# Optimization experiments

Measured on AMD Instinct MI355X. Metric: run time of the kernel, lower is better.

## Reference

```python
import jax, jax.numpy as jnp
import numpy as np

B, S, D, H, DK, FF = 2, 2048, 1024, 16, 64, 4096
EPS = 1e-6


def _layernorm(x, g, b):
    m = jnp.mean(x, axis=-1, keepdims=True)
    v = jnp.mean((x - m) ** 2, axis=-1, keepdims=True)
    return (x - m) * jax.lax.rsqrt(v + EPS) * g + b


def setup_inputs() -> dict:
    key = jax.random.key(0)
    ks = jax.random.split(key, 20)
    sc = 0.02
    rn = lambda k, sh: (jax.random.normal(k, sh, jnp.float32) * sc)
    return {
        "inputs": jax.random.normal(ks[0], (B, S, D), jnp.float32),
        "wq": rn(ks[1], (D, H * DK)), "bq": jnp.zeros((H * DK,), jnp.float32),
        "wk": rn(ks[2], (D, H * DK)), "bk": jnp.zeros((H * DK,), jnp.float32),
        "wv": rn(ks[3], (D, H * DK)), "bv": jnp.zeros((H * DK,), jnp.float32),
        "wo": rn(ks[4], (H * DK, D)), "bo": jnp.zeros((D,), jnp.float32),
        "ln1_g": jnp.ones((D,), jnp.float32), "ln1_b": jnp.zeros((D,), jnp.float32),
        "wi0": rn(ks[5], (D, FF)), "bi0": jnp.zeros((FF,), jnp.float32),
        "wi1": rn(ks[6], (D, FF)), "bi1": jnp.zeros((FF,), jnp.float32),
        "wff": rn(ks[7], (FF, D)), "bff": jnp.zeros((D,), jnp.float32),
        "ln2_g": jnp.ones((D,), jnp.float32), "ln2_b": jnp.zeros((D,), jnp.float32),
    }


def reference(inputs, wq, bq, wk, bk, wv, bv, wo, bo, ln1_g, ln1_b,
              wi0, bi0, wi1, bi1, wff, bff, ln2_g, ln2_b):
    # --- pre-norm MHA block ---
    h = _layernorm(inputs, ln1_g, ln1_b)
    q = (h @ wq + bq).reshape(B, S, H, DK)
    k = (h @ wk + bk).reshape(B, S, H, DK)
    v = (h @ wv + bv).reshape(B, S, H, DK)
    scores = jnp.einsum('bqhd,bkhd->bhqk', q, k) / jnp.sqrt(jnp.float32(DK))
    attn = jax.nn.softmax(scores, axis=-1)                 # [B,H,S,S]
    ctx = jnp.einsum('bhqk,bkhd->bqhd', attn, v).reshape(B, S, H * DK)
    h1 = inputs + (ctx @ wo + bo)
    # --- pre-norm GeGLU FFN block ---
    h2 = _layernorm(h1, ln2_g, ln2_b)
    hg = jax.nn.gelu(h2 @ wi0 + bi0, approximate=False)
    hl = h2 @ wi1 + bi1
    out = h1 + ((hg * hl) @ wff + bff)
    return out, attn
```

## Files before the change

### kernel.cpp

```cpp
#include <hip/hip_runtime.h>
#include <hip/hip_bf16.h>
#include <cstdint>

#define DEV __device__ __forceinline__

typedef __bf16 bf16_t;
typedef __bf16 bf16x8 __attribute__((ext_vector_type(8)));
typedef __bf16 bf16x4 __attribute__((ext_vector_type(4)));
typedef float  f32x4  __attribute__((ext_vector_type(4)));

constexpr int Bb = 2, Ss = 2048, Dd = 1024, Hh = 16, DKk = 64, FFf = 4096;
constexpr int TOK = Bb * Ss;
constexpr float LN_EPS = 1e-6f;

DEV void g2l16(const void* g, void* l) {
    __builtin_amdgcn_global_load_lds(
        (const __attribute__((address_space(1))) unsigned int*)g,
        (__attribute__((address_space(3))) unsigned int*)l, 16, 0, 0);
}

#define WAITCNT(N) asm volatile("s_waitcnt vmcnt(" #N ")" ::: "memory")
#define SCHEDB() __builtin_amdgcn_sched_barrier(0)

__global__ __launch_bounds__(256)
void transpose_all(const float* __restrict__ wq, const float* __restrict__ wk,
                   const float* __restrict__ wv, const float* __restrict__ wo,
                   const float* __restrict__ wi0, const float* __restrict__ wi1,
                   const float* __restrict__ wff,
                   bf16_t* wqT, bf16_t* wkT, bf16_t* wvT, bf16_t* woT,
                   bf16_t* wi0T, bf16_t* wi1T, bf16_t* wffT) {
    __shared__ float t[32][33];
    const int id = blockIdx.x;
    const float* src; bf16_t* dst; int K, N, tt;
    if (id < 4096) {
        const int w = id >> 10; tt = id & 1023; K = 1024; N = 1024;
        src = w == 0 ? wq : w == 1 ? wk : w == 2 ? wv : wo;
        dst = w == 0 ? wqT : w == 1 ? wkT : w == 2 ? wvT : woT;
    } else if (id < 12288) {
        const int w = (id - 4096) >> 12; tt = (id - 4096) & 4095; K = 1024; N = 4096;
        src = w ? wi1 : wi0; dst = w ? wi1T : wi0T;
    } else {
        tt = id - 12288; K = 4096; N = 1024;
        src = wff; dst = wffT;
    }
    const int ntn = N >> 5;
    const int n0 = (tt % ntn) * 32, k0 = (tt / ntn) * 32;
    const int tx = threadIdx.x & 31, ty = threadIdx.x >> 5;
#pragma unroll
    for (int i = 0; i < 4; ++i)
        t[ty + 8 * i][tx] = src[(size_t)(k0 + ty + 8 * i) * N + n0 + tx];
    __syncthreads();
#pragma unroll
    for (int i = 0; i < 4; ++i)
        dst[(size_t)(n0 + ty + 8 * i) * K + k0 + tx] = (bf16_t)t[tx][ty + 8 * i];
}

__global__ __launch_bounds__(256)
void concat3(const float* __restrict__ a, const float* __restrict__ b,
             const float* __restrict__ c, float* __restrict__ o) {
    const int i = blockIdx.x * 256 + threadIdx.x;
    o[i] = a[i]; o[1024 + i] = b[i]; o[2048 + i] = c[i];
}

__global__ __launch_bounds__(256)
void ln_fwd(const float* __restrict__ x, const float* __restrict__ g,
            const float* __restrict__ b, bf16_t* __restrict__ out) {
    __shared__ float red[8];
    const int row = blockIdx.x, tid = threadIdx.x;
    const float4 v = ((const float4*)(x + (size_t)row * Dd))[tid];
    float s  = v.x + v.y + v.z + v.w;
    float sq = v.x * v.x + v.y * v.y + v.z * v.z + v.w * v.w;
#pragma unroll
    for (int o = 32; o; o >>= 1) { s += __shfl_xor(s, o); sq += __shfl_xor(sq, o); }
    if ((tid & 63) == 0) { red[tid >> 6] = s; red[4 + (tid >> 6)] = sq; }
    __syncthreads();
    s  = red[0] + red[1] + red[2] + red[3];
    sq = red[4] + red[5] + red[6] + red[7];
    const float mean = s * (1.f / Dd);
    const float var  = sq * (1.f / Dd) - mean * mean;
    const float rs   = rsqrtf(var + LN_EPS);
    const float4 gv = ((const float4*)g)[tid];
    const float4 bv = ((const float4*)b)[tid];
    bf16x4 o4;
    o4[0] = (bf16_t)((v.x - mean) * rs * gv.x + bv.x);
    o4[1] = (bf16_t)((v.y - mean) * rs * gv.y + bv.y);
    o4[2] = (bf16_t)((v.z - mean) * rs * gv.z + bv.z);
    o4[3] = (bf16_t)((v.w - mean) * rs * gv.w + bv.w);
    ((bf16x4*)(out + (size_t)row * Dd))[tid] = o4;
}

template <int EPI>
DEV void gemm_epi(float val, int gr, int gc, int N,
                  void* outp, void* out2, void* out3, const float* resid) {
    if constexpr (EPI == 0) {
        ((bf16_t*)outp)[(size_t)gr * N + gc] = (bf16_t)val;
    } else if constexpr (EPI == 1) {
        const size_t idx = (size_t)gr * N + gc;
        ((float*)outp)[idx] = val + resid[idx];
    } else {
        const int sel = gc >> 10, col = gc & 1023;
        if (sel == 0) {
            ((bf16_t*)outp)[(size_t)gr * 1024 + col] = (bf16_t)val;
        } else if (sel == 1) {
            ((bf16_t*)out2)[(size_t)gr * 1024 + col] = (bf16_t)val;
        } else {
            const int bb = gr >> 11, sS = gr & 2047;
            ((bf16_t*)out3)[((size_t)bb << 21) + ((size_t)col << 11) + sS] = (bf16_t)val;
        }
    }
}

template <int BM, int BN, int EPI>
__global__ __launch_bounds__(256)
void gemm_t(const bf16_t* __restrict__ A, const bf16_t* __restrict__ Bt,
            const float* __restrict__ bias, const float* __restrict__ resid,
            void* __restrict__ outp, void* __restrict__ out2,
            void* __restrict__ out3, int M, int N, int K) {
    constexpr int WM = BM / 2, WN = BN / 2;
    constexpr int MI = WM / 16, NI = WN / 16;
    constexpr int CA = BM / 32, CB = BN / 32;
    __shared__ bf16_t As[BM * 64];
    __shared__ bf16_t Bs[BN * 64];
    const int tid = threadIdx.x;
    const int lane = tid & 63;
    const int wave = tid >> 6;
    const int wr = wave >> 1, wc = wave & 1;
    const int m0 = blockIdx.y * BM, n0 = blockIdx.x * BN;
    const int lr = lane & 15, lg = lane >> 4;

    const f32x4 z0 = {0.f, 0.f, 0.f, 0.f};
    f32x4 acc[MI][NI];
#pragma unroll
    for (int i = 0; i < MI; ++i)
#pragma unroll
        for (int j = 0; j < NI; ++j) acc[i][j] = z0;

    for (int k0 = 0; k0 < K; k0 += 64) {
#pragma unroll
        for (int c = 0; c < CA; ++c) {
            const int lin = c * 256 + tid;
            const int row = lin >> 3, col = (lin & 7) * 8;
            g2l16(A + (size_t)(m0 + row) * K + k0 + col, (char*)As + lin * 16);
        }
#pragma unroll
        for (int c = 0; c < CB; ++c) {
            const int lin = c * 256 + tid;
            const int row = lin >> 3, col = (lin & 7) * 8;
            g2l16(Bt + (size_t)(n0 + row) * K + k0 + col, (char*)Bs + lin * 16);
        }
        __syncthreads();

        bf16x8 af[2][MI], bw[2][NI];
#pragma unroll
        for (int kk = 0; kk < 2; ++kk)
#pragma unroll
            for (int mi = 0; mi < MI; ++mi)
                af[kk][mi] = *(const bf16x8*)(As + (wr * WM + mi * 16 + lr) * 64 +
                                              kk * 32 + lg * 8);
#pragma unroll
        for (int kk = 0; kk < 2; ++kk)
#pragma unroll
            for (int ni = 0; ni < NI; ++ni)
                bw[kk][ni] = *(const bf16x8*)(Bs + (wc * WN + ni * 16 + lr) * 64 +
                                              kk * 32 + lg * 8);
#pragma unroll
        for (int mi = 0; mi < MI; ++mi)
#pragma unroll
            for (int ni = 0; ni < NI; ++ni) {
                acc[mi][ni] = __builtin_amdgcn_mfma_f32_16x16x32_bf16(
                    af[0][mi], bw[0][ni], acc[mi][ni], 0, 0, 0);
                acc[mi][ni] = __builtin_amdgcn_mfma_f32_16x16x32_bf16(
                    af[1][mi], bw[1][ni], acc[mi][ni], 0, 0, 0);
            }
        __syncthreads();
    }

#pragma unroll
    for (int mi = 0; mi < MI; ++mi)
#pragma unroll
        for (int ni = 0; ni < NI; ++ni) {
            const int gc = n0 + wc * WN + ni * 16 + lr;
            const int gr0 = m0 + wr * WM + mi * 16 + lg * 4;
            const float bvl = bias[gc];
#pragma unroll
            for (int r = 0; r < 4; ++r)
                gemm_epi<EPI>(acc[mi][ni][r] + bvl, gr0 + r, gc, N, outp, out2, out3, resid);
        }
}

__global__ __launch_bounds__(256)
void gemm_geglu(const bf16_t* __restrict__ A, const bf16_t* __restrict__ Bg,
                const bf16_t* __restrict__ Bl, const float* __restrict__ bi0,
                const float* __restrict__ bi1, bf16_t* __restrict__ gout) {
    __shared__ bf16_t As[128 * 64];
    __shared__ bf16_t Bgs[64 * 64];
    __shared__ bf16_t Bls[64 * 64];
    const int tid = threadIdx.x;
    const int lane = tid & 63;
    const int wave = tid >> 6;
    const int wr = wave >> 1, wc = wave & 1;
    const int m0 = blockIdx.y * 128, n0 = blockIdx.x * 64;
    const int lr = lane & 15, lg = lane >> 4;

    const f32x4 z0 = {0.f, 0.f, 0.f, 0.f};
    f32x4 ag[4][2], al[4][2];
#pragma unroll
    for (int i = 0; i < 4; ++i)
#pragma unroll
        for (int j = 0; j < 2; ++j) { ag[i][j] = z0; al[i][j] = z0; }

    for (int k0 = 0; k0 < 1024; k0 += 64) {
#pragma unroll
        for (int c = 0; c < 4; ++c) {
            const int lin = c * 256 + tid;
            const int row = lin >> 3, col = (lin & 7) * 8;
            g2l16(A + (size_t)(m0 + row) * 1024 + k0 + col, (char*)As + lin * 16);
        }
#pragma unroll
        for (int c = 0; c < 2; ++c) {
            const int lin = c * 256 + tid;
            const int row = lin >> 3, col = (lin & 7) * 8;
            g2l16(Bg + (size_t)(n0 + row) * 1024 + k0 + col, (char*)Bgs + lin * 16);
        }
#pragma unroll
        for (int c = 0; c < 2; ++c) {
            const int lin = c * 256 + tid;
            const int row = lin >> 3, col = (lin & 7) * 8;
            g2l16(Bl + (size_t)(n0 + row) * 1024 + k0 + col, (char*)Bls + lin * 16);
        }
        __syncthreads();

        bf16x8 af[2][4], bg[2][2], bl[2][2];
#pragma unroll
        for (int kk = 0; kk < 2; ++kk) {
#pragma unroll
            for (int mi = 0; mi < 4; ++mi)
                af[kk][mi] = *(const bf16x8*)(As + (wr * 64 + mi * 16 + lr) * 64 +
                                              kk * 32 + lg * 8);
#pragma unroll
            for (int ni = 0; ni < 2; ++ni) {
                bg[kk][ni] = *(const bf16x8*)(Bgs + (wc * 32 + ni * 16 + lr) * 64 +
                                              kk * 32 + lg * 8);
                bl[kk][ni] = *(const bf16x8*)(Bls + (wc * 32 + ni * 16 + lr) * 64 +
                                              kk * 32 + lg * 8);
            }
        }
#pragma unroll
        for (int mi = 0; mi < 4; ++mi)
#pragma unroll
            for (int ni = 0; ni < 2; ++ni) {
#pragma unroll
                for (int kk = 0; kk < 2; ++kk) {
                    ag[mi][ni] = __builtin_amdgcn_mfma_f32_16x16x32_bf16(
                        af[kk][mi], bg[kk][ni], ag[mi][ni], 0, 0, 0);
                    al[mi][ni] = __builtin_amdgcn_mfma_f32_16x16x32_bf16(
                        af[kk][mi], bl[kk][ni], al[mi][ni], 0, 0, 0);
                }
            }
        __syncthreads();
    }

#pragma unroll
    for (int mi = 0; mi < 4; ++mi)
#pragma unroll
        for (int ni = 0; ni < 2; ++ni) {
            const int gc = n0 + wc * 32 + ni * 16 + lr;
            const int gr0 = m0 + wr * 64 + mi * 16 + lg * 4;
            const float b0 = bi0[gc], b1 = bi1[gc];
#pragma unroll
            for (int r = 0; r < 4; ++r) {
                const float x = ag[mi][ni][r] + b0;
                const float y = al[mi][ni][r] + b1;
                const float ge = 0.5f * x * (1.f + erff(x * 0.70710678118654752f));
                gout[(size_t)(gr0 + r) * 4096 + gc] = (bf16_t)(ge * y);
            }
        }
}

__global__ __launch_bounds__(256)
void attn_fused(const bf16_t* __restrict__ q, const bf16_t* __restrict__ k,
                const bf16_t* __restrict__ vT, float* __restrict__ attn,
                bf16_t* __restrict__ ctx) {
    __shared__ bf16_t Ks[3][64 * 64];
    __shared__ bf16_t Vs[3][64 * 64];
    const int tid = threadIdx.x, lane = tid & 63, wave = tid >> 6;
    const int lr = lane & 15, lg = lane >> 4;
    int blk = blockIdx.x;
    blk = (blk & 7) * 128 + (blk >> 3);
    const int qc = blk & 31, bh = blk >> 5;
    const int b = bh >> 4, h = bh & 15;
    const int q0 = qc * 64 + wave * 16;
    const size_t base = (size_t)b * (Ss * 1024) + h * 64;
    constexpr float SCL = 0.125f * 1.4426950408889634f;
    const f32x4 z0 = {0.f, 0.f, 0.f, 0.f};

    const int st_r8 = lane >> 3;
    const int st_c0 = (lane & 7) ^ (st_r8 & 3);

    const bf16x8 aq0 = *(const bf16x8*)(q + base + (size_t)(q0 + lr) * 1024 + lg * 8);
    const bf16x8 aq1 = *(const bf16x8*)(q + base + (size_t)(q0 + lr) * 1024 + 32 + lg * 8);
    const bf16_t* kb = k + base;
    const bf16_t* vb_base = vT + ((size_t)bh * 64) * Ss;

#define STAGE_K(kt_, buf_)                                                        \
    {                                                                             \
        _Pragma("unroll")                                                         \
        for (int i = 0; i < 2; ++i)                                               \
            g2l16(kb + (size_t)((kt_) * 64 + wave * 16 + i * 8 + st_r8) * 1024 +  \
                      (st_c0 ^ (i * 4)) * 8,                                      \
                  &Ks[buf_][wave * 1024 + i * 512]);                              \
    }
#define STAGE_V(kt_, buf_)                                                        \
    {                                                                             \
        _Pragma("unroll")                                                         \
        for (int i = 0; i < 2; ++i)                                               \
            g2l16(vb_base + (size_t)(wave * 16 + i * 8 + st_r8) * Ss +            \
                      (kt_) * 64 + (st_c0 ^ (i * 4)) * 8,                         \
                  &Vs[buf_][wave * 1024 + i * 512]);                              \
    }

    f32x4 ea = z0, eb = z0;
    STAGE_K(0, 0);
    STAGE_K(1, 1);
    for (int kt = 0; kt < 32; ++kt) {
        const int buf = kt % 3;
        if (kt == 31) { WAITCNT(0); } else { WAITCNT(2); }
        SCHEDB();
        __builtin_amdgcn_s_barrier();
        SCHEDB();
        f32x4 sa[4];
        __builtin_amdgcn_s_setprio(1);
#pragma unroll
        for (int ct = 0; ct < 4; ++ct) {
            const int ar = ct * 16 + lr;
            const int hz = (ar & 3) | (((ar >> 3) & 1) << 2);
            bf16x8 k0 = *(const bf16x8*)&Ks[buf][ar * 64 + (lg ^ hz) * 8];
            bf16x8 k1 = *(const bf16x8*)&Ks[buf][ar * 64 + (((4 + lg) ^ hz)) * 8];
            sa[ct] = __builtin_amdgcn_mfma_f32_16x16x32_bf16(k0, aq0, z0, 0, 0, 0);
            sa[ct] = __builtin_amdgcn_mfma_f32_16x16x32_bf16(k1, aq1, sa[ct], 0, 0, 0);
        }
        __builtin_amdgcn_s_setprio(0);
#pragma unroll
        for (int r = 0; r < 4; ++r) {
            ea[r] += exp2f(sa[0][r] * SCL) + exp2f(sa[1][r] * SCL);
            eb[r] += exp2f(sa[2][r] * SCL) + exp2f(sa[3][r] * SCL);
        }
        if (kt + 2 < 32) STAGE_K(kt + 2, (kt + 2) % 3);
    }
    float e = ((ea[0] + ea[1]) + (ea[2] + ea[3])) + ((eb[0] + eb[1]) + (eb[2] + eb[3]));
    e += __shfl_xor(e, 16);
    e += __shfl_xor(e, 32);
    const float invl = 1.f / e;

    f32x4 cacc[4];
#pragma unroll
    for (int nd = 0; nd < 4; ++nd) cacc[nd] = z0;

    float* attn_base = attn + ((size_t)bh * Ss + q0 + lr) * Ss;

    __builtin_amdgcn_s_barrier();
    SCHEDB();

    STAGE_K(0, 0); STAGE_V(0, 0);
    STAGE_K(1, 1); STAGE_V(1, 1);
    for (int kt = 0; kt < 32; ++kt) {
        const int buf = kt % 3;
        if (kt == 0 || kt == 31) { WAITCNT(4); } else { WAITCNT(8); }
        SCHEDB();
        __builtin_amdgcn_s_barrier();
        SCHEDB();
#pragma unroll
        for (int kp = 0; kp < 2; ++kp) {
            bf16x8 pa;
            __builtin_amdgcn_s_setprio(1);
#pragma unroll
            for (int ch = 0; ch < 2; ++ch) {
                const int pr = kp * 32 + (lr >> 2) * 8 + ch * 4 + (lr & 3);
                const int hz = (pr & 3) | (((pr >> 3) & 1) << 2);
                bf16x8 k0 = *(const bf16x8*)&Ks[buf][pr * 64 + (lg ^ hz) * 8];
                bf16x8 k1 = *(const bf16x8*)&Ks[buf][pr * 64 + (((4 + lg) ^ hz)) * 8];
                f32x4 sb = __builtin_amdgcn_mfma_f32_16x16x32_bf16(k0, aq0, z0, 0, 0, 0);
                sb = __builtin_amdgcn_mfma_f32_16x16x32_bf16(k1, aq1, sb, 0, 0, 0);
                float4 p;
                p.x = exp2f(sb[0] * SCL) * invl;
                p.y = exp2f(sb[1] * SCL) * invl;
                p.z = exp2f(sb[2] * SCL) * invl;
                p.w = exp2f(sb[3] * SCL) * invl;
                *(float4*)(attn_base + kt * 64 + kp * 32 + lg * 8 + ch * 4) = p;
                pa[ch * 4 + 0] = (bf16_t)p.x;
                pa[ch * 4 + 1] = (bf16_t)p.y;
                pa[ch * 4 + 2] = (bf16_t)p.z;
                pa[ch * 4 + 3] = (bf16_t)p.w;
            }
#pragma unroll
            for (int nd = 0; nd < 4; ++nd) {
                const int vr = nd * 16 + lr;
                const int hv = (vr & 3) | (((vr >> 3) & 1) << 2);
                bf16x8 vb = *(const bf16x8*)&Vs[buf][vr * 64 + (((kp * 4 + lg) ^ hv)) * 8];
                cacc[nd] = __builtin_amdgcn_mfma_f32_16x16x32_bf16(pa, vb, cacc[nd], 0, 0, 0);
            }
            __builtin_amdgcn_s_setprio(0);
        }
        if (kt + 2 < 32) {
            const int nb = (kt + 2) % 3;
            STAGE_K(kt + 2, nb);
            STAGE_V(kt + 2, nb);
        }
    }
#pragma unroll
    for (int nd = 0; nd < 4; ++nd)
#pragma unroll
        for (int r = 0; r < 4; ++r)
            ctx[((size_t)b * Ss + q0 + lg * 4 + r) * 1024 + h * 64 + nd * 16 + lr] =
                (bf16_t)cacc[nd][r];
#undef STAGE_K
#undef STAGE_V
}

extern "C" void kernel_launch(void* const* d_in, const int* in_sizes, int n_in,
                              void* d_out, int out_size, void* d_ws, size_t ws_size,
                              hipStream_t stream) {
    const float* inp  = (const float*)d_in[0];
    const float* wq   = (const float*)d_in[1];
    const float* bq   = (const float*)d_in[2];
    const float* wk   = (const float*)d_in[3];
    const float* bk   = (const float*)d_in[4];
    const float* wv   = (const float*)d_in[5];
    const float* bv   = (const float*)d_in[6];
    const float* wo   = (const float*)d_in[7];
    const float* bo   = (const float*)d_in[8];
    const float* ln1g = (const float*)d_in[9];
    const float* ln1b = (const float*)d_in[10];
    const float* wi0  = (const float*)d_in[11];
    const float* bi0  = (const float*)d_in[12];
    const float* wi1  = (const float*)d_in[13];
    const float* bi1  = (const float*)d_in[14];
    const float* wff  = (const float*)d_in[15];
    const float* bff  = (const float*)d_in[16];
    const float* ln2g = (const float*)d_in[17];
    const float* ln2b = (const float*)d_in[18];

    const size_t M1 = 1u << 20;
    bf16_t* wsb  = (bf16_t*)d_ws;
    bf16_t* wqT  = wsb + 0 * M1;
    bf16_t* wkT  = wsb + 1 * M1;
    bf16_t* wvT  = wsb + 2 * M1;
    bf16_t* woT  = wsb + 3 * M1;
    bf16_t* wi0T = wsb + 4 * M1;
    bf16_t* wi1T = wsb + 8 * M1;
    bf16_t* wffT = wsb + 12 * M1;
    bf16_t* hbuf = wsb + 16 * M1;
    bf16_t* qbuf = wsb + 20 * M1;
    bf16_t* kbuf = wsb + 24 * M1;
    bf16_t* vTb  = wsb + 28 * M1;
    bf16_t* ctxb = wsb + 32 * M1;
    float*  h1   = (float*)(wsb + 36 * M1);
    bf16_t* gbuf = wsb + 44 * M1;
    float*  cb   = (float*)(wsb + 60 * M1);

    float* out  = (float*)d_out;
    float* attn = out + (size_t)TOK * Dd;

    transpose_all<<<16384, 256, 0, stream>>>(wq, wk, wv, wo, wi0, wi1, wff,
                                             wqT, wkT, wvT, woT, wi0T, wi1T, wffT);

    concat3<<<4, 256, 0, stream>>>(bq, bk, bv, cb);

    ln_fwd<<<TOK, 256, 0, stream>>>(inp, ln1g, ln1b, hbuf);

    gemm_t<128, 128, 3><<<dim3(24, 32), 256, 0, stream>>>(hbuf, wqT, cb, nullptr,
                                                          qbuf, kbuf, vTb, TOK, 3072, 1024);

    attn_fused<<<Bb * Hh * (Ss / 64), 256, 0, stream>>>(qbuf, kbuf, vTb, attn, ctxb);

    gemm_t<64, 64, 1><<<dim3(16, 64), 256, 0, stream>>>(ctxb, woT, bo, inp, h1,
                                                        nullptr, nullptr, TOK, 1024, 1024);

    ln_fwd<<<TOK, 256, 0, stream>>>(h1, ln2g, ln2b, hbuf);

    gemm_geglu<<<dim3(64, 32), 256, 0, stream>>>(hbuf, wi0T, wi1T, bi0, bi1, gbuf);

    gemm_t<64, 64, 1><<<dim3(16, 64), 256, 0, stream>>>(gbuf, wffT, bff, h1, out,
                                                        nullptr, nullptr, TOK, 1024, 4096);
}
```

Measured before the change: 510.3 us.

## Split-K the FFN down-projection and widen attention blocks to 128 queries

The final FFN GEMM (K=4096) is now split into two K halves using a 128x64 tile and a z grid dimension. Each half writes fp32 partials, and a separate reduce kernel adds the partials, the residual and the bias. Separately, the attention kernel now runs 8 waves per block covering 128 query rows, so each staged K/V tile is shared by twice as many queries and each thread issues fewer loads. The trade-offs are extra fp32 partial traffic plus one more launch, and higher per-block register and LDS pressure in attention.

```diff
diff --git a/kernel.cpp b/kernel.cpp
--- a/kernel.cpp
+++ b/kernel.cpp
@@ -90,13 +90,15 @@
 }
 
 template <int EPI>
-DEV void gemm_epi(float val, int gr, int gc, int N,
+DEV void gemm_epi(float val, int gr, int gc, int N, size_t zofs,
                   void* outp, void* out2, void* out3, const float* resid) {
     if constexpr (EPI == 0) {
         ((bf16_t*)outp)[(size_t)gr * N + gc] = (bf16_t)val;
     } else if constexpr (EPI == 1) {
         const size_t idx = (size_t)gr * N + gc;
         ((float*)outp)[idx] = val + resid[idx];
+    } else if constexpr (EPI == 4) {
+        ((float*)outp)[zofs + (size_t)gr * N + gc] = val;
     } else {
         const int sel = gc >> 10, col = gc & 1023;
         if (sel == 0) {
@@ -115,7 +117,7 @@
 void gemm_t(const bf16_t* __restrict__ A, const bf16_t* __restrict__ Bt,
             const float* __restrict__ bias, const float* __restrict__ resid,
             void* __restrict__ outp, void* __restrict__ out2,
-            void* __restrict__ out3, int M, int N, int K) {
+            void* __restrict__ out3, int M, int N, int K, int ld) {
     constexpr int WM = BM / 2, WN = BN / 2;
     constexpr int MI = WM / 16, NI = WN / 16;
     constexpr int CA = BM / 32, CB = BN / 32;
@@ -126,6 +128,8 @@
     const int wave = tid >> 6;
     const int wr = wave >> 1, wc = wave & 1;
     const int m0 = blockIdx.y * BM, n0 = blockIdx.x * BN;
+    const int koff = blockIdx.z * K;
+    const size_t zofs = (size_t)blockIdx.z * M * N;
     const int lr = lane & 15, lg = lane >> 4;
 
     const f32x4 z0 = {0.f, 0.f, 0.f, 0.f};
@@ -140,13 +144,13 @@
         for (int c = 0; c < CA; ++c) {
             const int lin = c * 256 + tid;
             const int row = lin >> 3, col = (lin & 7) * 8;
-            g2l16(A + (size_t)(m0 + row) * K + k0 + col, (char*)As + lin * 16);
+            g2l16(A + (size_t)(m0 + row) * ld + koff + k0 + col, (char*)As + lin * 16);
         }
 #pragma unroll
         for (int c = 0; c < CB; ++c) {
             const int lin = c * 256 + tid;
             const int row = lin >> 3, col = (lin & 7) * 8;
-            g2l16(Bt + (size_t)(n0 + row) * K + k0 + col, (char*)Bs + lin * 16);
+            g2l16(Bt + (size_t)(n0 + row) * ld + koff + k0 + col, (char*)Bs + lin * 16);
         }
         __syncthreads();
 
@@ -181,11 +185,29 @@
         for (int ni = 0; ni < NI; ++ni) {
             const int gc = n0 + wc * WN + ni * 16 + lr;
             const int gr0 = m0 + wr * WM + mi * 16 + lg * 4;
-            const float bvl = bias[gc];
+            const float bvl = (EPI == 4) ? 0.f : bias[gc];
 #pragma unroll
             for (int r = 0; r < 4; ++r)
-                gemm_epi<EPI>(acc[mi][ni][r] + bvl, gr0 + r, gc, N, outp, out2, out3, resid);
-        }
+                gemm_epi<EPI>(acc[mi][ni][r] + bvl, gr0 + r, gc, N, zofs,
+                              outp, out2, out3, resid);
+        }
+}
+
+__global__ __launch_bounds__(256)
+void reduce2(const float* __restrict__ part, const float* __restrict__ h1,
+             const float* __restrict__ bff, float* __restrict__ out) {
+    const int row = blockIdx.x, tid = threadIdx.x;
+    const size_t idx = (size_t)row * 1024 + tid * 4;
+    const float4 a = *(const float4*)(part + idx);
+    const float4 b = *(const float4*)(part + (size_t)4096 * 1024 + idx);
+    const float4 r = *(const float4*)(h1 + idx);
+    const float4 bv = *(const float4*)(bff + tid * 4);
+    float4 o;
+    o.x = a.x + b.x + r.x + bv.x;
+    o.y = a.y + b.y + r.y + bv.y;
+    o.z = a.z + b.z + r.z + bv.z;
+    o.w = a.w + b.w + r.w + bv.w;
+    *(float4*)(out + idx) = o;
 }
 
 __global__ __launch_bounds__(256)
@@ -277,7 +299,7 @@
         }
 }
 
-__global__ __launch_bounds__(256)
+__global__ __launch_bounds__(512)
 void attn_fused(const bf16_t* __restrict__ q, const bf16_t* __restrict__ k,
                 const bf16_t* __restrict__ vT, float* __restrict__ attn,
                 bf16_t* __restrict__ ctx) {
@@ -286,45 +308,36 @@
     const int tid = threadIdx.x, lane = tid & 63, wave = tid >> 6;
     const int lr = lane & 15, lg = lane >> 4;
     int blk = blockIdx.x;
-    blk = (blk & 7) * 128 + (blk >> 3);
-    const int qc = blk & 31, bh = blk >> 5;
+    blk = (blk & 7) * 64 + (blk >> 3);
+    const int qc = blk & 15, bh = blk >> 4;
     const int b = bh >> 4, h = bh & 15;
-    const int q0 = qc * 64 + wave * 16;
+    const int q0 = qc * 128 + wave * 16;
     const size_t base = (size_t)b * (Ss * 1024) + h * 64;
     constexpr float SCL = 0.125f * 1.4426950408889634f;
     const f32x4 z0 = {0.f, 0.f, 0.f, 0.f};
 
     const int st_r8 = lane >> 3;
-    const int st_c0 = (lane & 7) ^ (st_r8 & 3);
+    const int st_row = wave * 8 + st_r8;
+    const int st_c0 = (lane & 7) ^ (st_r8 & 3) ^ ((wave & 1) << 2);
 
     const bf16x8 aq0 = *(const bf16x8*)(q + base + (size_t)(q0 + lr) * 1024 + lg * 8);
     const bf16x8 aq1 = *(const bf16x8*)(q + base + (size_t)(q0 + lr) * 1024 + 32 + lg * 8);
     const bf16_t* kb = k + base;
     const bf16_t* vb_base = vT + ((size_t)bh * 64) * Ss;
 
-#define STAGE_K(kt_, buf_)                                                        \
-    {                                                                             \
-        _Pragma("unroll")                                                         \
-        for (int i = 0; i < 2; ++i)                                               \
-            g2l16(kb + (size_t)((kt_) * 64 + wave * 16 + i * 8 + st_r8) * 1024 +  \
-                      (st_c0 ^ (i * 4)) * 8,                                      \
-                  &Ks[buf_][wave * 1024 + i * 512]);                              \
-    }
-#define STAGE_V(kt_, buf_)                                                        \
-    {                                                                             \
-        _Pragma("unroll")                                                         \
-        for (int i = 0; i < 2; ++i)                                               \
-            g2l16(vb_base + (size_t)(wave * 16 + i * 8 + st_r8) * Ss +            \
-                      (kt_) * 64 + (st_c0 ^ (i * 4)) * 8,                         \
-                  &Vs[buf_][wave * 1024 + i * 512]);                              \
-    }
+#define STAGE_K(kt_, buf_)                                                       \
+    g2l16(kb + (size_t)((kt_) * 64 + st_row) * 1024 + st_c0 * 8,                 \
+          &Ks[buf_][wave * 512]);
+#define STAGE_V(kt_, buf_)                                                       \
+    g2l16(vb_base + (size_t)st_row * Ss + (kt_) * 64 + st_c0 * 8,                \
+          &Vs[buf_][wave * 512]);
 
     f32x4 ea = z0, eb = z0;
     STAGE_K(0, 0);
     STAGE_K(1, 1);
     for (int kt = 0; kt < 32; ++kt) {
         const int buf = kt % 3;
-        if (kt == 31) { WAITCNT(0); } else { WAITCNT(2); }
+        if (kt == 31) { WAITCNT(0); } else { WAITCNT(1); }
         SCHEDB();
         __builtin_amdgcn_s_barrier();
         SCHEDB();
@@ -365,7 +378,9 @@
     STAGE_K(1, 1); STAGE_V(1, 1);
     for (int kt = 0; kt < 32; ++kt) {
         const int buf = kt % 3;
-        if (kt == 0 || kt == 31) { WAITCNT(4); } else { WAITCNT(8); }
+        if (kt == 0) { WAITCNT(2); }
+        else if (kt == 31) { WAITCNT(4); }
+        else { WAITCNT(6); }
         SCHEDB();
         __builtin_amdgcn_s_barrier();
         SCHEDB();
@@ -456,6 +471,7 @@
     bf16_t* ctxb = wsb + 32 * M1;
     float*  h1   = (float*)(wsb + 36 * M1);
     bf16_t* gbuf = wsb + 44 * M1;
+    float*  part = (float*)(wsb + 20 * M1);
     float*  cb   = (float*)(wsb + 60 * M1);
 
     float* out  = (float*)d_out;
@@ -468,18 +484,20 @@
 
     ln_fwd<<<TOK, 256, 0, stream>>>(inp, ln1g, ln1b, hbuf);
 
-    gemm_t<128, 128, 3><<<dim3(24, 32), 256, 0, stream>>>(hbuf, wqT, cb, nullptr,
-                                                          qbuf, kbuf, vTb, TOK, 3072, 1024);
-
-    attn_fused<<<Bb * Hh * (Ss / 64), 256, 0, stream>>>(qbuf, kbuf, vTb, attn, ctxb);
-
-    gemm_t<64, 64, 1><<<dim3(16, 64), 256, 0, stream>>>(ctxb, woT, bo, inp, h1,
-                                                        nullptr, nullptr, TOK, 1024, 1024);
+    gemm_t<128, 128, 3><<<dim3(24, 32), 256, 0, stream>>>(
+        hbuf, wqT, cb, nullptr, qbuf, kbuf, vTb, TOK, 3072, 1024, 1024);
+
+    attn_fused<<<Bb * Hh * (Ss / 128), 512, 0, stream>>>(qbuf, kbuf, vTb, attn, ctxb);
+
+    gemm_t<64, 64, 1><<<dim3(16, 64), 256, 0, stream>>>(
+        ctxb, woT, bo, inp, h1, nullptr, nullptr, TOK, 1024, 1024, 1024);
 
     ln_fwd<<<TOK, 256, 0, stream>>>(h1, ln2g, ln2b, hbuf);
 
     gemm_geglu<<<dim3(64, 32), 256, 0, stream>>>(hbuf, wi0T, wi1T, bi0, bi1, gbuf);
 
-    gemm_t<64, 64, 1><<<dim3(16, 64), 256, 0, stream>>>(gbuf, wffT, bff, h1, out,
-                                                        nullptr, nullptr, TOK, 1024, 4096);
-}
+    gemm_t<128, 64, 4><<<dim3(16, 32, 2), 256, 0, stream>>>(
+        gbuf, wffT, bff, nullptr, part, nullptr, nullptr, TOK, 1024, 2048, 4096);
+
+    reduce2<<<4096, 256, 0, stream>>>(part, h1, bff, out);
+}
```

Result: faster. 478.0 us (-6.3%).
